# Optimization experiments

Hardware: AMD Instinct MI355X
Metric: run time of the kernel (lower is better)

The kernel has to match this reference:

```python
import jax, jax.numpy as jnp
import numpy as np

NUM_EXPERTS = 16
TOP_K = 2
AUX_LOSS_COEF = 0.01


def setup_inputs() -> dict:
    key = jax.random.key(0)
    ks = jax.random.split(key, 5)
    B, S, D, I, E = 4, 2048, 1024, 2816, NUM_EXPERTS
    scale = 0.02
    return {
        "x": jax.random.normal(ks[0], (B, S, D), dtype=jnp.float32),
        "gate_w": jax.random.normal(ks[1], (D, E), dtype=jnp.float32) * scale,
        "Wg": jax.random.normal(ks[2], (E, D, I), dtype=jnp.float32) * scale,
        "Wu": jax.random.normal(ks[3], (E, D, I), dtype=jnp.float32) * scale,
        "Wd": jax.random.normal(ks[4], (E, I, D), dtype=jnp.float32) * scale,
    }


def _moe_forward(x, gate_w, Wg, Wu, Wd):
    B, S, D = x.shape
    E = gate_w.shape[1]
    # Router
    logits = x @ gate_w                      # [B,S,E]
    probs = jax.nn.softmax(logits, axis=-1)  # [B,S,E]
    topk_w, topk_idx = jax.lax.top_k(probs, TOP_K)        # [B,S,K]
    topk_w = topk_w / jnp.sum(topk_w, axis=-1, keepdims=True)
    # Per-token combine weight for each expert: [B,S,E]
    onehot = jax.nn.one_hot(topk_idx, E, dtype=x.dtype)   # [B,S,K,E]
    combine_w = jnp.einsum("bsk,bske->bse", topk_w, onehot)
    x_flat = x.reshape(-1, D)                # [T,D]
    w_flat = combine_w.reshape(-1, E)        # [T,E]
    # Accumulate weighted expert outputs (loop over fixed small E; unselected
    # tokens get zero weight, identical math to masked gather/scatter).
    out = jnp.zeros_like(x_flat)
    for e in range(E):
        h = jax.nn.silu(x_flat @ Wg[e]) * (x_flat @ Wu[e])  # [T,I]
        out = out + (h @ Wd[e]) * w_flat[:, e:e + 1]
    out = out.reshape(B, S, D)
    # Load balancing aux loss
    expert_mask = onehot.sum(axis=2)                        # [B,S,E]
    tokens_per_expert = expert_mask.mean(axis=(0, 1))       # [E]
    router_prob_per_expert = probs.mean(axis=(0, 1))        # [E]
    aux_loss = AUX_LOSS_COEF * jnp.sum(tokens_per_expert * router_prob_per_expert) * E
    return out, aux_loss


def reference(x, gate_w, Wg, Wu, Wd):
    return _moe_forward(x, gate_w, Wg, Wu, Wd)
```

## Files before the change

kernel.cpp:

```cpp
#include <hip/hip_runtime.h>
#include <stdint.h>

#define T_TOKENS 8192
#define D_DIM 1024
#define I_DIM 2816
#define E_NUM 16
#define N_SLOTS 16384

typedef float f32x4 __attribute__((ext_vector_type(4)));
typedef short s16x8 __attribute__((ext_vector_type(8)));
typedef short s16x4 __attribute__((ext_vector_type(4)));
typedef unsigned short u16;
typedef unsigned int u32;

__device__ __forceinline__ u16 f2bf(float f) {
  u32 u = __builtin_bit_cast(u32, f);
  u = (u + 0x7FFFu + ((u >> 16) & 1u)) >> 16;
  return (u16)u;
}
__device__ __forceinline__ float bf2f(u16 h) {
  u32 u = ((u32)h) << 16;
  return __builtin_bit_cast(float, u);
}
__device__ __forceinline__ u32 pack2(float a, float b) {
  return (u32)f2bf(a) | ((u32)f2bf(b) << 16);
}
__device__ __forceinline__ void async_load16(const void* g, void* l) {
  __builtin_amdgcn_global_load_lds(
      (const __attribute__((address_space(1))) void*)g,
      (__attribute__((address_space(3))) void*)l, 16, 0, 0);
}

__global__ void router_kernel(const float* __restrict__ x,
                              const float* __restrict__ gw,
                              int* __restrict__ e12, float* __restrict__ w12,
                              int* __restrict__ cnt, float* __restrict__ probsum) {
  __shared__ float sProb[E_NUM];
  __shared__ int sCnt[E_NUM];
  int tid = threadIdx.x;
  if (tid < E_NUM) { sProb[tid] = 0.f; sCnt[tid] = 0; }
  __syncthreads();
  int g = tid >> 4, i = tid & 15;
  int t = blockIdx.x * 16 + g;
  float acc[E_NUM];
#pragma unroll
  for (int e = 0; e < E_NUM; e++) acc[e] = 0.f;
  const f32x4* x4 = (const f32x4*)(x + (size_t)t * D_DIM);
  const f32x4* g4 = (const f32x4*)gw;
  for (int jj = 0; jj < 16; jj++) {
    f32x4 xv = x4[i + 16 * jj];
    int jb = 4 * (i + 16 * jj);
#pragma unroll
    for (int r = 0; r < 4; r++) {
      float xs = xv[r];
#pragma unroll
      for (int e4 = 0; e4 < 4; e4++) {
        f32x4 gv = g4[(jb + r) * 4 + e4];
        acc[e4 * 4 + 0] += xs * gv[0];
        acc[e4 * 4 + 1] += xs * gv[1];
        acc[e4 * 4 + 2] += xs * gv[2];
        acc[e4 * 4 + 3] += xs * gv[3];
      }
    }
  }
#pragma unroll
  for (int e = 0; e < E_NUM; e++) {
    float v = acc[e];
    v += __shfl_down(v, 8, 16);
    v += __shfl_down(v, 4, 16);
    v += __shfl_down(v, 2, 16);
    v += __shfl_down(v, 1, 16);
    acc[e] = v;
  }
  if (i == 0) {
    float mx = acc[0];
#pragma unroll
    for (int e = 1; e < E_NUM; e++) mx = fmaxf(mx, acc[e]);
    float p[E_NUM]; float s = 0.f;
#pragma unroll
    for (int e = 0; e < E_NUM; e++) { p[e] = __expf(acc[e] - mx); s += p[e]; }
    float inv = 1.f / s;
#pragma unroll
    for (int e = 0; e < E_NUM; e++) p[e] *= inv;
    int e1 = 0; float p1 = p[0];
#pragma unroll
    for (int e = 1; e < E_NUM; e++) if (p[e] > p1) { p1 = p[e]; e1 = e; }
    int e2 = (e1 == 0) ? 1 : 0; float p2 = p[e2];
#pragma unroll
    for (int e = 0; e < E_NUM; e++) if (e != e1 && p[e] > p2) { p2 = p[e]; e2 = e; }
    float wsum = p1 + p2;
    e12[2 * t] = e1; e12[2 * t + 1] = e2;
    w12[2 * t] = p1 / wsum; w12[2 * t + 1] = p2 / wsum;
#pragma unroll
    for (int e = 0; e < E_NUM; e++) atomicAdd(&sProb[e], p[e]);
    atomicAdd(&sCnt[e1], 1);
    atomicAdd(&sCnt[e2], 1);
  }
  __syncthreads();
  if (tid < E_NUM) {
    atomicAdd(&cnt[tid], sCnt[tid]);
    atomicAdd(&probsum[tid], sProb[tid]);
  }
}

__global__ void prefix_kernel(const int* __restrict__ cnt, int* __restrict__ offsets) {
  if (threadIdx.x == 0) {
    int s = 0;
    for (int e = 0; e < E_NUM; e++) { offsets[e] = s; s += cnt[e]; }
    offsets[E_NUM] = s;
  }
}

__global__ void build_kernel(const int* __restrict__ e12, const float* __restrict__ w12,
                             const int* __restrict__ offsets, int* __restrict__ cursor,
                             int* __restrict__ tlist, float* __restrict__ wlist) {
  int t = blockIdx.x * 256 + threadIdx.x;
  if (t >= T_TOKENS) return;
#pragma unroll
  for (int k = 0; k < 2; k++) {
    int e = e12[2 * t + k];
    int pos = atomicAdd(&cursor[e], 1);
    int idx = offsets[e] + pos;
    tlist[idx] = t;
    wlist[idx] = w12[2 * t + k];
  }
}

__global__ void gather_kernel(const float* __restrict__ x, const int* __restrict__ tlist,
                              u16* __restrict__ Xe) {
  int r = blockIdx.x * 4 + (threadIdx.x >> 6);
  int lane = threadIdx.x & 63;
  int tok = tlist[r];
  const f32x4* src = (const f32x4*)(x + (size_t)tok * D_DIM);
  u32* dst = (u32*)(Xe + (size_t)r * D_DIM);
#pragma unroll
  for (int c = 0; c < 4; c++) {
    f32x4 v = src[lane + 64 * c];
    dst[(lane + 64 * c) * 2] = pack2(v[0], v[1]);
    dst[(lane + 64 * c) * 2 + 1] = pack2(v[2], v[3]);
  }
}

template <int MODE, int KDIM, int NDIM>
__global__ __launch_bounds__(256) void gemm_kernel(
    const u16* __restrict__ Abuf, const float* __restrict__ Bw,
    u16* __restrict__ Hbuf, float* __restrict__ out,
    const int* __restrict__ cnt, const int* __restrict__ offsets,
    const int* __restrict__ tlist, const float* __restrict__ wlist) {
  int e = blockIdx.z;
  int Me = cnt[e];
  int m0 = blockIdx.y * 128;
  if (m0 >= Me) return;
  int n0 = blockIdx.x * 128;
  int rowBase = offsets[e];
  const float* Be = Bw + (size_t)e * KDIM * NDIM;

  __shared__ u16 Ash[128 * 32];
  __shared__ u16 Bsh[128 * 36];

  int tid = threadIdx.x;
  int lane = tid & 63;
  int wv = tid >> 6;
  int mq = wv & 1, nq = wv >> 1;
  int lrow = lane & 15, lq = lane >> 4;
  int tmod = tid & 31, tdiv = tid >> 5;

  f32x4 acc[4][4];
#pragma unroll
  for (int a = 0; a < 4; a++)
#pragma unroll
    for (int b = 0; b < 4; b++) acc[a][b] = (f32x4)0.f;

  for (int k0 = 0; k0 < KDIM; k0 += 32) {
#pragma unroll
    for (int rep = 0; rep < 2; rep++) {
      int idx = tid + 256 * rep;
      int row = idx >> 2, q = idx & 3;
      int gr = m0 + row;
      gr = (gr < Me) ? gr : (Me - 1);
      const u16* gsrc = Abuf + (size_t)(rowBase + gr) * KDIM + k0 + q * 8;
      async_load16(gsrc, &Ash[(wv * 64 + 256 * rep) * 8]);
    }
#pragma unroll
    for (int rep = 0; rep < 2; rep++) {
      int k = 2 * (tdiv + rep * 8);
      const float* b0 = Be + (size_t)(k0 + k) * NDIM + n0;
      const float* b1 = b0 + NDIM;
#pragma unroll
      for (int ii = 0; ii < 4; ii++) {
        int n = tmod + ii * 32;
        *(u32*)&Bsh[n * 36 + k] = pack2(b0[n], b1[n]);
      }
    }
    __syncthreads();
    s16x8 af[4], bfr[4];
#pragma unroll
    for (int fm = 0; fm < 4; fm++)
      af[fm] = *(const s16x8*)&Ash[(mq * 64 + fm * 16 + lrow) * 32 + lq * 8];
#pragma unroll
    for (int fn = 0; fn < 4; fn++) {
      const u16* bp = &Bsh[(nq * 64 + fn * 16 + lrow) * 36 + lq * 8];
      s16x4 lo = *(const s16x4*)bp;
      s16x4 hi = *(const s16x4*)(bp + 4);
      bfr[fn] = __builtin_shufflevector(lo, hi, 0, 1, 2, 3, 4, 5, 6, 7);
    }
#pragma unroll
    for (int fm = 0; fm < 4; fm++)
#pragma unroll
      for (int fn = 0; fn < 4; fn++)
        acc[fm][fn] = __builtin_amdgcn_mfma_f32_16x16x32_bf16(af[fm], bfr[fn], acc[fm][fn], 0, 0, 0);
    __syncthreads();
  }
#pragma unroll
  for (int fm = 0; fm < 4; fm++) {
#pragma unroll
    for (int i = 0; i < 4; i++) {
      int m = m0 + mq * 64 + fm * 16 + lq * 4 + i;
      if (m >= Me) continue;
      size_t arow = (size_t)(rowBase + m);
#pragma unroll
      for (int fn = 0; fn < 4; fn++) {
        int col = n0 + nq * 64 + fn * 16 + lrow;
        float v = acc[fm][fn][i];
        if (MODE == 0) {
          float sg = v / (1.f + __expf(-v));
          Hbuf[arow * I_DIM + col] = f2bf(sg);
        } else if (MODE == 1) {
          size_t hx = arow * I_DIM + col;
          float gg = bf2f(Hbuf[hx]);
          Hbuf[hx] = f2bf(gg * v);
        } else {
          int tok = tlist[arow];
          float w = wlist[arow];
          atomicAdd(&out[(size_t)tok * D_DIM + col], v * w);
        }
      }
    }
  }
}

__global__ void aux_kernel(const int* __restrict__ cnt, const float* __restrict__ probsum,
                           float* __restrict__ aux_out) {
  if (threadIdx.x == 0) {
    float s = 0.f;
    for (int e = 0; e < E_NUM; e++) s += (float)cnt[e] * probsum[e];
    aux_out[0] = 0.01f * 16.f * s / (8192.f * 8192.f);
  }
}

extern "C" void kernel_launch(void* const* d_in, const int* in_sizes, int n_in,
                              void* d_out, int out_size, void* d_ws, size_t ws_size,
                              hipStream_t stream) {
  const float* x  = (const float*)d_in[0];
  const float* gw = (const float*)d_in[1];
  const float* Wg = (const float*)d_in[2];
  const float* Wu = (const float*)d_in[3];
  const float* Wd = (const float*)d_in[4];
  float* outf = (float*)d_out;
  char* ws = (char*)d_ws;
  int*   cnt     = (int*)(ws + 0);
  int*   cursor  = (int*)(ws + 64);
  float* probsum = (float*)(ws + 128);
  int*   offsets = (int*)(ws + 192);
  int*   e12     = (int*)(ws + 512);
  float* w12     = (float*)(ws + 66048);
  int*   tlist   = (int*)(ws + 131584);
  float* wlist   = (float*)(ws + 197120);
  u16*   Xe      = (u16*)(ws + (1 << 20));
  u16*   H       = (u16*)(ws + 34603008);

  hipMemsetAsync(d_out, 0, (size_t)(T_TOKENS * D_DIM + 1) * sizeof(float), stream);
  hipMemsetAsync(d_ws, 0, 512, stream);

  router_kernel<<<512, 256, 0, stream>>>(x, gw, e12, w12, cnt, probsum);
  prefix_kernel<<<1, 64, 0, stream>>>(cnt, offsets);
  build_kernel<<<32, 256, 0, stream>>>(e12, w12, offsets, cursor, tlist, wlist);
  gather_kernel<<<4096, 256, 0, stream>>>(x, tlist, Xe);

  gemm_kernel<0, D_DIM, I_DIM><<<dim3(22, 64, E_NUM), 256, 0, stream>>>(
      Xe, Wg, H, outf, cnt, offsets, tlist, wlist);
  gemm_kernel<1, D_DIM, I_DIM><<<dim3(22, 64, E_NUM), 256, 0, stream>>>(
      Xe, Wu, H, outf, cnt, offsets, tlist, wlist);
  gemm_kernel<2, I_DIM, D_DIM><<<dim3(8, 64, E_NUM), 256, 0, stream>>>(
      H, Wd, H, outf, cnt, offsets, tlist, wlist);

  aux_kernel<<<1, 64, 0, stream>>>(cnt, probsum, outf + (size_t)(T_TOKENS * D_DIM));
}
```

Baseline: 1.271 ms.

## Pre-transpose weights to bf16 and fuse gate/up GEMMs

Adds a transpose kernel that converts each expert's fp32 weights into a bf16 N-major layout, so the GEMMs can stream B tiles with async global-to-LDS loads instead of converting fp32 inside every tile. The gate and up projections are fused into one kernel that shares the A tile and applies SiLU·up in its epilogue, which removes the read-modify-write pass over H. The aux loss is folded into the prefix kernel. The transposes cost an extra read and write of all weights on every call, plus extra workspace, and the fused kernel holds twice as many accumulators, which raises register pressure.

```diff
diff --git a/kernel.cpp b/kernel.cpp
--- a/kernel.cpp
+++ b/kernel.cpp
@@ -17,10 +17,6 @@
   u32 u = __builtin_bit_cast(u32, f);
   u = (u + 0x7FFFu + ((u >> 16) & 1u)) >> 16;
   return (u16)u;
-}
-__device__ __forceinline__ float bf2f(u16 h) {
-  u32 u = ((u32)h) << 16;
-  return __builtin_bit_cast(float, u);
 }
 __device__ __forceinline__ u32 pack2(float a, float b) {
   return (u32)f2bf(a) | ((u32)f2bf(b) << 16);
@@ -103,11 +99,15 @@
   }
 }
 
-__global__ void prefix_kernel(const int* __restrict__ cnt, int* __restrict__ offsets) {
+__global__ void prefix_kernel(const int* __restrict__ cnt, int* __restrict__ offsets,
+                              const float* __restrict__ probsum, float* __restrict__ aux_out) {
   if (threadIdx.x == 0) {
     int s = 0;
     for (int e = 0; e < E_NUM; e++) { offsets[e] = s; s += cnt[e]; }
     offsets[E_NUM] = s;
+    float a = 0.f;
+    for (int e = 0; e < E_NUM; e++) a += (float)cnt[e] * probsum[e];
+    aux_out[0] = 0.01f * 16.f * a / (8192.f * 8192.f);
   }
 }
 
@@ -141,10 +141,120 @@
   }
 }
 
-template <int MODE, int KDIM, int NDIM>
-__global__ __launch_bounds__(256) void gemm_kernel(
-    const u16* __restrict__ Abuf, const float* __restrict__ Bw,
-    u16* __restrict__ Hbuf, float* __restrict__ out,
+template <int K, int N>
+__global__ __launch_bounds__(256) void transpose_kernel(const float* __restrict__ W,
+                                                        u16* __restrict__ Wt) {
+  __shared__ u16 tile[64][66];
+  int e = blockIdx.z;
+  int k0 = blockIdx.x * 64;
+  int n0 = blockIdx.y * 64;
+  const float* Win = W + (size_t)e * K * N;
+  u16* Wout = Wt + (size_t)e * N * K;
+  int t = threadIdx.x;
+  int r = t >> 4;
+  int c4 = (t & 15) * 4;
+#pragma unroll
+  for (int rep = 0; rep < 4; rep++) {
+    int k = r + rep * 16;
+    f32x4 v = *(const f32x4*)(Win + (size_t)(k0 + k) * N + n0 + c4);
+    *(u32*)&tile[k][c4] = pack2(v[0], v[1]);
+    *(u32*)&tile[k][c4 + 2] = pack2(v[2], v[3]);
+  }
+  __syncthreads();
+#pragma unroll
+  for (int rep = 0; rep < 4; rep++) {
+    int n = r + rep * 16;
+    int k4 = c4;
+    s16x4 o;
+    o[0] = tile[k4 + 0][n];
+    o[1] = tile[k4 + 1][n];
+    o[2] = tile[k4 + 2][n];
+    o[3] = tile[k4 + 3][n];
+    *(s16x4*)(Wout + (size_t)(n0 + n) * K + k0 + k4) = o;
+  }
+}
+
+__global__ __launch_bounds__(256, 2) void gemm_gu_kernel(
+    const u16* __restrict__ Abuf, const u16* __restrict__ Bg, const u16* __restrict__ Bu,
+    u16* __restrict__ Hbuf,
+    const int* __restrict__ cnt, const int* __restrict__ offsets) {
+  int e = blockIdx.z;
+  int Me = cnt[e];
+  int m0 = blockIdx.y * 128;
+  if (m0 >= Me) return;
+  int n0 = blockIdx.x * 128;
+  int rowBase = offsets[e];
+  const u16* Bge = Bg + (size_t)e * I_DIM * D_DIM;
+  const u16* Bue = Bu + (size_t)e * I_DIM * D_DIM;
+
+  __shared__ u16 Ash[128 * 32];
+  __shared__ u16 Bgsh[128 * 32];
+  __shared__ u16 Bush[128 * 32];
+
+  int tid = threadIdx.x;
+  int lane = tid & 63;
+  int wv = tid >> 6;
+  int mq = wv & 1, nq = wv >> 1;
+  int lrow = lane & 15, lq = lane >> 4;
+
+  f32x4 accg[4][4], accu[4][4];
+#pragma unroll
+  for (int a = 0; a < 4; a++)
+#pragma unroll
+    for (int b = 0; b < 4; b++) { accg[a][b] = (f32x4)0.f; accu[a][b] = (f32x4)0.f; }
+
+  for (int k0 = 0; k0 < D_DIM; k0 += 32) {
+#pragma unroll
+    for (int rep = 0; rep < 2; rep++) {
+      int idx = tid + 256 * rep;
+      int row = idx >> 2, q = idx & 3;
+      int ldso = (wv * 64 + 256 * rep) * 8;
+      int gr = m0 + row;
+      gr = (gr < Me) ? gr : (Me - 1);
+      async_load16(Abuf + (size_t)(rowBase + gr) * D_DIM + k0 + q * 8, &Ash[ldso]);
+      async_load16(Bge + (size_t)(n0 + row) * D_DIM + k0 + q * 8, &Bgsh[ldso]);
+      async_load16(Bue + (size_t)(n0 + row) * D_DIM + k0 + q * 8, &Bush[ldso]);
+    }
+    __syncthreads();
+    s16x8 af[4], bg[4], bu[4];
+#pragma unroll
+    for (int fm = 0; fm < 4; fm++)
+      af[fm] = *(const s16x8*)&Ash[(mq * 64 + fm * 16 + lrow) * 32 + lq * 8];
+#pragma unroll
+    for (int fn = 0; fn < 4; fn++) {
+      bg[fn] = *(const s16x8*)&Bgsh[(nq * 64 + fn * 16 + lrow) * 32 + lq * 8];
+      bu[fn] = *(const s16x8*)&Bush[(nq * 64 + fn * 16 + lrow) * 32 + lq * 8];
+    }
+#pragma unroll
+    for (int fm = 0; fm < 4; fm++)
+#pragma unroll
+      for (int fn = 0; fn < 4; fn++) {
+        accg[fm][fn] = __builtin_amdgcn_mfma_f32_16x16x32_bf16(af[fm], bg[fn], accg[fm][fn], 0, 0, 0);
+        accu[fm][fn] = __builtin_amdgcn_mfma_f32_16x16x32_bf16(af[fm], bu[fn], accu[fm][fn], 0, 0, 0);
+      }
+    __syncthreads();
+  }
+#pragma unroll
+  for (int fm = 0; fm < 4; fm++) {
+#pragma unroll
+    for (int i = 0; i < 4; i++) {
+      int m = m0 + mq * 64 + fm * 16 + lq * 4 + i;
+      if (m >= Me) continue;
+      size_t arow = (size_t)(rowBase + m);
+#pragma unroll
+      for (int fn = 0; fn < 4; fn++) {
+        int col = n0 + nq * 64 + fn * 16 + lrow;
+        float g = accg[fm][fn][i];
+        float u = accu[fm][fn][i];
+        float h = (g / (1.f + __expf(-g))) * u;
+        Hbuf[arow * I_DIM + col] = f2bf(h);
+      }
+    }
+  }
+}
+
+__global__ __launch_bounds__(256) void gemm_down_kernel(
+    const u16* __restrict__ Abuf, const u16* __restrict__ Bd, float* __restrict__ out,
     const int* __restrict__ cnt, const int* __restrict__ offsets,
     const int* __restrict__ tlist, const float* __restrict__ wlist) {
   int e = blockIdx.z;
@@ -153,17 +263,16 @@
   if (m0 >= Me) return;
   int n0 = blockIdx.x * 128;
   int rowBase = offsets[e];
-  const float* Be = Bw + (size_t)e * KDIM * NDIM;
+  const u16* Bde = Bd + (size_t)e * D_DIM * I_DIM;
 
   __shared__ u16 Ash[128 * 32];
-  __shared__ u16 Bsh[128 * 36];
+  __shared__ u16 Bsh[128 * 32];
 
   int tid = threadIdx.x;
   int lane = tid & 63;
   int wv = tid >> 6;
   int mq = wv & 1, nq = wv >> 1;
   int lrow = lane & 15, lq = lane >> 4;
-  int tmod = tid & 31, tdiv = tid >> 5;
 
   f32x4 acc[4][4];
 #pragma unroll
@@ -171,26 +280,16 @@
 #pragma unroll
     for (int b = 0; b < 4; b++) acc[a][b] = (f32x4)0.f;
 
-  for (int k0 = 0; k0 < KDIM; k0 += 32) {
+  for (int k0 = 0; k0 < I_DIM; k0 += 32) {
 #pragma unroll
     for (int rep = 0; rep < 2; rep++) {
       int idx = tid + 256 * rep;
       int row = idx >> 2, q = idx & 3;
+      int ldso = (wv * 64 + 256 * rep) * 8;
       int gr = m0 + row;
       gr = (gr < Me) ? gr : (Me - 1);
-      const u16* gsrc = Abuf + (size_t)(rowBase + gr) * KDIM + k0 + q * 8;
-      async_load16(gsrc, &Ash[(wv * 64 + 256 * rep) * 8]);
-    }
-#pragma unroll
-    for (int rep = 0; rep < 2; rep++) {
-      int k = 2 * (tdiv + rep * 8);
-      const float* b0 = Be + (size_t)(k0 + k) * NDIM + n0;
-      const float* b1 = b0 + NDIM;
-#pragma unroll
-      for (int ii = 0; ii < 4; ii++) {
-        int n = tmod + ii * 32;
-        *(u32*)&Bsh[n * 36 + k] = pack2(b0[n], b1[n]);
-      }
+      async_load16(Abuf + (size_t)(rowBase + gr) * I_DIM + k0 + q * 8, &Ash[ldso]);
+      async_load16(Bde + (size_t)(n0 + row) * I_DIM + k0 + q * 8, &Bsh[ldso]);
     }
     __syncthreads();
     s16x8 af[4], bfr[4];
@@ -198,12 +297,8 @@
     for (int fm = 0; fm < 4; fm++)
       af[fm] = *(const s16x8*)&Ash[(mq * 64 + fm * 16 + lrow) * 32 + lq * 8];
 #pragma unroll
-    for (int fn = 0; fn < 4; fn++) {
-      const u16* bp = &Bsh[(nq * 64 + fn * 16 + lrow) * 36 + lq * 8];
-      s16x4 lo = *(const s16x4*)bp;
-      s16x4 hi = *(const s16x4*)(bp + 4);
-      bfr[fn] = __builtin_shufflevector(lo, hi, 0, 1, 2, 3, 4, 5, 6, 7);
-    }
+    for (int fn = 0; fn < 4; fn++)
+      bfr[fn] = *(const s16x8*)&Bsh[(nq * 64 + fn * 16 + lrow) * 32 + lq * 8];
 #pragma unroll
     for (int fm = 0; fm < 4; fm++)
 #pragma unroll
@@ -218,33 +313,14 @@
       int m = m0 + mq * 64 + fm * 16 + lq * 4 + i;
       if (m >= Me) continue;
       size_t arow = (size_t)(rowBase + m);
+      int tok = tlist[arow];
+      float w = wlist[arow];
 #pragma unroll
       for (int fn = 0; fn < 4; fn++) {
         int col = n0 + nq * 64 + fn * 16 + lrow;
-        float v = acc[fm][fn][i];
-        if (MODE == 0) {
-          float sg = v / (1.f + __expf(-v));
-          Hbuf[arow * I_DIM + col] = f2bf(sg);
-        } else if (MODE == 1) {
-          size_t hx = arow * I_DIM + col;
-          float gg = bf2f(Hbuf[hx]);
-          Hbuf[hx] = f2bf(gg * v);
-        } else {
-          int tok = tlist[arow];
-          float w = wlist[arow];
-          atomicAdd(&out[(size_t)tok * D_DIM + col], v * w);
-        }
+        atomicAdd(&out[(size_t)tok * D_DIM + col], acc[fm][fn][i] * w);
       }
     }
-  }
-}
-
-__global__ void aux_kernel(const int* __restrict__ cnt, const float* __restrict__ probsum,
-                           float* __restrict__ aux_out) {
-  if (threadIdx.x == 0) {
-    float s = 0.f;
-    for (int e = 0; e < E_NUM; e++) s += (float)cnt[e] * probsum[e];
-    aux_out[0] = 0.01f * 16.f * s / (8192.f * 8192.f);
   }
 }
 
@@ -268,21 +344,23 @@
   float* wlist   = (float*)(ws + 197120);
   u16*   Xe      = (u16*)(ws + (1 << 20));
   u16*   H       = (u16*)(ws + 34603008);
+  u16*   WtA     = (u16*)(ws + 134217728);
+  u16*   WtB     = (u16*)(ws + 234881024);
 
   hipMemsetAsync(d_out, 0, (size_t)(T_TOKENS * D_DIM + 1) * sizeof(float), stream);
   hipMemsetAsync(d_ws, 0, 512, stream);
 
   router_kernel<<<512, 256, 0, stream>>>(x, gw, e12, w12, cnt, probsum);
-  prefix_kernel<<<1, 64, 0, stream>>>(cnt, offsets);
+  prefix_kernel<<<1, 64, 0, stream>>>(cnt, offsets, probsum, outf + (size_t)(T_TOKENS * D_DIM));
   build_kernel<<<32, 256, 0, stream>>>(e12, w12, offsets, cursor, tlist, wlist);
   gather_kernel<<<4096, 256, 0, stream>>>(x, tlist, Xe);
 
-  gemm_kernel<0, D_DIM, I_DIM><<<dim3(22, 64, E_NUM), 256, 0, stream>>>(
-      Xe, Wg, H, outf, cnt, offsets, tlist, wlist);
-  gemm_kernel<1, D_DIM, I_DIM><<<dim3(22, 64, E_NUM), 256, 0, stream>>>(
-      Xe, Wu, H, outf, cnt, offsets, tlist, wlist);
-  gemm_kernel<2, I_DIM, D_DIM><<<dim3(8, 64, E_NUM), 256, 0, stream>>>(
-      H, Wd, H, outf, cnt, offsets, tlist, wlist);
-
-  aux_kernel<<<1, 64, 0, stream>>>(cnt, probsum, outf + (size_t)(T_TOKENS * D_DIM));
-}
+  transpose_kernel<D_DIM, I_DIM><<<dim3(16, 44, E_NUM), 256, 0, stream>>>(Wg, WtA);
+  transpose_kernel<D_DIM, I_DIM><<<dim3(16, 44, E_NUM), 256, 0, stream>>>(Wu, WtB);
+
+  gemm_gu_kernel<<<dim3(22, 64, E_NUM), 256, 0, stream>>>(Xe, WtA, WtB, H, cnt, offsets);
+
+  transpose_kernel<I_DIM, D_DIM><<<dim3(44, 16, E_NUM), 256, 0, stream>>>(Wd, WtA);
+
+  gemm_down_kernel<<<dim3(8, 64, E_NUM), 256, 0, stream>>>(H, WtA, outf, cnt, offsets, tlist, wlist);
+}
```

New measurement: 1.132 ms. 10.9% less time.
